# Kernel optimization log

Hardware: AMD Instinct MI355X
Metric: run time of the kernel (lower is better)

## Reference

```python
import jax, jax.numpy as jnp
import numpy as np

T, D, I, E, K = 2048, 2048, 5632, 8, 2


def setup_inputs() -> dict:
    key = jax.random.key(0)
    k1, k2, k3, k4, k5 = jax.random.split(key, 5)
    s = 0.02
    return {
        "x": jax.random.normal(k1, (T, D), dtype=jnp.float32),
        "gate_w": jax.random.normal(k2, (E, D), dtype=jnp.float32) * s,
        "w_gate": jax.random.normal(k3, (E, I, D), dtype=jnp.float32) * s,
        "w_up": jax.random.normal(k4, (E, I, D), dtype=jnp.float32) * s,
        "w_down": jax.random.normal(k5, (E, D, I), dtype=jnp.float32) * s,
    }


def reference(x, gate_w, w_gate, w_up, w_down):
    # Router: logits [T, E], top-k then softmax over the k selected logits
    logits = x @ gate_w.T
    top_vals, top_idx = jax.lax.top_k(logits, K)          # [T, K]
    rw = jax.nn.softmax(top_vals, axis=-1)                # [T, K]
    # Dense combine weights [T, E]: sum of routing weights over selected slots.
    # Mathematically identical to the per-(expert, slot) scatter-add in torch,
    # since duplicate selections of the same expert just sum their weights.
    combine = jnp.sum(jax.nn.one_hot(top_idx, E, dtype=x.dtype) * rw[..., None], axis=1)  # [T, E]
    # SwiGLU expert MLPs, batched over experts (grouped GEMM as dense einsum)
    g = jnp.einsum("td,eid->tei", x, w_gate)              # [T, E, I]
    u = jnp.einsum("td,eid->tei", x, w_up)                # [T, E, I]
    h = jax.nn.silu(g) * u                                 # [T, E, I]
    out_e = jnp.einsum("tei,edi->ted", h, w_down)         # [T, E, D]
    return jnp.einsum("ted,te->td", out_e, combine)       # [T, D]
```

## Files before the change

kernel.cpp:

```cpp
#include <hip/hip_runtime.h>
#include <hip/hip_bf16.h>
#include <stdint.h>

#define TTOK 2048
#define DDIM 2048
#define IDIM 5632
#define NEXP 8

typedef __attribute__((ext_vector_type(8))) short bf16x8;
typedef __attribute__((ext_vector_type(4))) float f32x4;
typedef __attribute__((ext_vector_type(8))) unsigned short u16x8;
typedef __attribute__((ext_vector_type(4))) unsigned short u16x4;

__device__ __forceinline__ unsigned short f2bf(float f) {
  union { float f; uint32_t u; } v; v.f = f;
  uint32_t u = v.u + 0x7fffu + ((v.u >> 16) & 1u);
  return (unsigned short)(u >> 16);
}

__device__ __forceinline__ uint32_t fbits(float f) {
  union { float f; uint32_t u; } v; v.f = f; return v.u;
}

__device__ __forceinline__ u16x8 cvt8t(float4 a, float4 b) {
  union { u16x8 v; uint32_t w[4]; } r;
  r.w[0] = __builtin_amdgcn_perm(fbits(a.y), fbits(a.x), 0x07060302);
  r.w[1] = __builtin_amdgcn_perm(fbits(a.w), fbits(a.z), 0x07060302);
  r.w[2] = __builtin_amdgcn_perm(fbits(b.y), fbits(b.x), 0x07060302);
  r.w[3] = __builtin_amdgcn_perm(fbits(b.w), fbits(b.z), 0x07060302);
  return r.v;
}

typedef __attribute__((address_space(3))) void lds_t;
typedef const __attribute__((address_space(1))) void gbl_t;
__device__ __forceinline__ void gload16(const void* g, void* l) {
  __builtin_amdgcn_global_load_lds((gbl_t*)g, (lds_t*)l, 16, 0, 0);
}

#define PIPE_BAR1() asm volatile("s_waitcnt vmcnt(12) lgkmcnt(0)\n\ts_barrier" ::: "memory")
#define PIPE_BAR2() asm volatile("s_barrier" ::: "memory")

__global__ __launch_bounds__(256) void router_kernel(
    const float* __restrict__ x, const float* __restrict__ gw,
    unsigned short* __restrict__ xbf,
    int* __restrict__ cnt, int* __restrict__ slots, float* __restrict__ wts)
{
  const int lane = threadIdx.x & 63;
  const int t = (blockIdx.x * blockDim.x + threadIdx.x) >> 6;
  const float* xr = x + (size_t)t * DDIM;
  float acc[NEXP];
#pragma unroll
  for (int e = 0; e < NEXP; ++e) acc[e] = 0.f;
#pragma unroll
  for (int it = 0; it < DDIM / 256; ++it) {
    const int d = (it * 64 + lane) * 4;
    const float4 xv = *(const float4*)(xr + d);
    u16x4 xb; xb[0]=f2bf(xv.x); xb[1]=f2bf(xv.y); xb[2]=f2bf(xv.z); xb[3]=f2bf(xv.w);
    *(u16x4*)(xbf + (size_t)t * DDIM + d) = xb;
#pragma unroll
    for (int e = 0; e < NEXP; ++e) {
      const float4 gv = *(const float4*)(gw + (size_t)e * DDIM + d);
      acc[e] += xv.x*gv.x + xv.y*gv.y + xv.z*gv.z + xv.w*gv.w;
    }
  }
#pragma unroll
  for (int e = 0; e < NEXP; ++e) {
    float v = acc[e];
#pragma unroll
    for (int off = 32; off > 0; off >>= 1) v += __shfl_xor(v, off);
    acc[e] = v;
  }
  if (lane == 0) {
    int i0 = 0; float v0 = acc[0];
#pragma unroll
    for (int e = 1; e < NEXP; ++e) if (acc[e] > v0) { v0 = acc[e]; i0 = e; }
    int i1 = -1; float v1 = -3.4e38f;
#pragma unroll
    for (int e = 0; e < NEXP; ++e) { if (e == i0) continue; if (acc[e] > v1) { v1 = acc[e]; i1 = e; } }
    const float e1 = __expf(v1 - v0);
    const float w0 = 1.f / (1.f + e1);
    const float w1 = e1 / (1.f + e1);
    const int p0 = atomicAdd(&cnt[i0], 1);
    slots[i0 * TTOK + p0] = t * 2;     wts[i0 * TTOK + p0] = w0;
    const int p1 = atomicAdd(&cnt[i1], 1);
    slots[i1 * TTOK + p1] = t * 2 + 1; wts[i1 * TTOK + p1] = w1;
  }
}

__global__ void plan_kernel(const int* __restrict__ cnt,
                            int* __restrict__ tilemap, int* __restrict__ ntiles)
{
  if (threadIdx.x == 0 && blockIdx.x == 0) {
    int n = 0;
#pragma unroll
    for (int e = 0; e < NEXP; ++e) {
      const int nt = (cnt[e] + 127) >> 7;
      for (int m = 0; m < nt; ++m) tilemap[n++] = (e << 8) | m;
    }
    ntiles[0] = n;
  }
}


__global__ __launch_bounds__(256) void gateup_kernel(
    const unsigned short* __restrict__ xbf,
    const float* __restrict__ wg, const float* __restrict__ wu,
    const int* __restrict__ cnt, const int* __restrict__ slots,
    const int* __restrict__ tilemap, const int* __restrict__ ntiles,
    unsigned short* __restrict__ h)
{
  const int flat = (blockIdx.x & 7) * 440 + (blockIdx.x >> 3);
  const int ti = flat % 40;
  if (ti >= ntiles[0]) return;
  const int em = tilemap[ti];
  const int e = em >> 8;
  const int mt = em & 255;
  const int n0 = (flat / 40) * 64;
  const int count = cnt[e];
  const int m0 = mt * 128;

  __shared__ unsigned short A[2][128][64];
  __shared__ unsigned short Bg[64][64];
  __shared__ unsigned short Bu[64][64];
  __shared__ int rslot[128];
  __shared__ int rtok[128];

  const int tid = threadIdx.x;
  const int lane = tid & 63;
  const int wid = tid >> 6;

  if (tid < 128) {
    const int idx = m0 + tid;
    const int safe = slots[e * TTOK + m0];
    const int s = (idx < count) ? slots[e * TTOK + idx] : safe;
    rslot[tid] = (idx < count) ? s : -1;
    rtok[tid] = s >> 1;
  }
  __syncthreads();

  const int aswz = ((lane & 7) ^ ((lane >> 3) & 7)) * 8;
  const unsigned short* aptr[4];
#pragma unroll
  for (int j = 0; j < 4; ++j) {
    const int arow = wid * 32 + j * 8 + (lane >> 3);
    aptr[j] = xbf + (size_t)rtok[arow] * DDIM + aswz;
  }

  const int brow = tid >> 2;
  const int bcb = (tid & 3) * 2;
  const int bswz = brow & 7;
  const size_t wboff = (size_t)e * IDIM * DDIM + (size_t)(n0 + brow) * DDIM + bcb * 8;
  const float* gsrc = wg + wboff;
  const float* usrc = wu + wboff;

  const int wr = wid >> 1, wc = wid & 1;
  const int fr = lane & 15;
  const int kc = lane >> 4;
  const int rsw = fr & 7;

  f32x4 accg[4][2] = {};
  f32x4 accu[4][2] = {};

#pragma unroll
  for (int j = 0; j < 4; ++j) gload16(aptr[j], &A[0][wid * 32][0] + j * 512);
  float4 pg4[4], pu4[4];
#pragma unroll
  for (int q = 0; q < 4; ++q) { pg4[q] = *(const float4*)(gsrc + q * 4); pu4[q] = *(const float4*)(usrc + q * 4); }

#pragma unroll 2
  for (int t = 0; t < 32; ++t) {
    const int cur = t & 1;
    const int kp = (t < 31) ? (t + 1) * 64 : 31 * 64;

#pragma unroll
    for (int j = 0; j < 4; ++j) gload16(aptr[j] + kp, &A[cur ^ 1][wid * 32][0] + j * 512);
    float4 ng4[4], nu4[4];
#pragma unroll
    for (int q = 0; q < 4; ++q) { ng4[q] = *(const float4*)(gsrc + kp + q * 4); nu4[q] = *(const float4*)(usrc + kp + q * 4); }
    __builtin_amdgcn_sched_barrier(0);
#pragma unroll
    for (int qq = 0; qq < 2; ++qq) {
      const int oc = ((bcb + qq) ^ bswz) * 8;
      *(u16x8*)&Bg[brow][oc] = cvt8t(pg4[qq * 2], pg4[qq * 2 + 1]);
      *(u16x8*)&Bu[brow][oc] = cvt8t(pu4[qq * 2], pu4[qq * 2 + 1]);
    }
    PIPE_BAR1();

    __builtin_amdgcn_s_setprio(1);
#pragma unroll
    for (int kk = 0; kk < 2; ++kk) {
      bf16x8 a[4], bg[2], bu[2];
      const int cs = ((kk * 4 + kc) ^ rsw) * 8;
#pragma unroll
      for (int mf = 0; mf < 4; ++mf)
        a[mf] = *(const bf16x8*)&A[cur][wr * 64 + mf * 16 + fr][cs];
#pragma unroll
      for (int nf = 0; nf < 2; ++nf) {
        bg[nf] = *(const bf16x8*)&Bg[wc * 32 + nf * 16 + fr][cs];
        bu[nf] = *(const bf16x8*)&Bu[wc * 32 + nf * 16 + fr][cs];
      }
#pragma unroll
      for (int mf = 0; mf < 4; ++mf)
#pragma unroll
        for (int nf = 0; nf < 2; ++nf) {
          accg[mf][nf] = __builtin_amdgcn_mfma_f32_16x16x32_bf16(a[mf], bg[nf], accg[mf][nf], 0, 0, 0);
          accu[mf][nf] = __builtin_amdgcn_mfma_f32_16x16x32_bf16(a[mf], bu[nf], accu[mf][nf], 0, 0, 0);
        }
    }
    __builtin_amdgcn_s_setprio(0);

    PIPE_BAR2();

#pragma unroll
    for (int q = 0; q < 4; ++q) { pg4[q] = ng4[q]; pu4[q] = nu4[q]; }
  }

#pragma unroll
  for (int mf = 0; mf < 4; ++mf)
#pragma unroll
    for (int nf = 0; nf < 2; ++nf)
#pragma unroll
      for (int j = 0; j < 4; ++j) {
        const int r = wr * 64 + mf * 16 + (lane >> 4) * 4 + j;
        const int s = rslot[r];
        if (s >= 0) {
          const float g = accg[mf][nf][j];
          const float u = accu[mf][nf][j];
          const float hv = g / (1.f + __expf(-g)) * u;
          h[(size_t)s * IDIM + n0 + wc * 32 + nf * 16 + fr] = f2bf(hv);
        }
      }
}

__global__ __launch_bounds__(256) void down_kernel(
    const unsigned short* __restrict__ h,
    const float* __restrict__ wd,
    const int* __restrict__ cnt, const int* __restrict__ slots,
    const float* __restrict__ wts,
    const int* __restrict__ tilemap, const int* __restrict__ ntiles,
    float* __restrict__ out)
{
  const int flat = (blockIdx.x & 7) * 160 + (blockIdx.x >> 3);
  const int ti = flat % 40;
  if (ti >= ntiles[0]) return;
  const int em = tilemap[ti];
  const int e = em >> 8;
  const int mt = em & 255;
  const int r2 = flat / 40;
  const int n0 = (r2 & 15) * 128;
  const int ks = r2 >> 4;
  const int kbase = ks * (IDIM / 2);
  const int count = cnt[e];
  const int m0 = mt * 128;

  __shared__ unsigned short A[2][128][64];
  __shared__ unsigned short B[128][64];
  __shared__ int rslot[128];
  __shared__ float rw[128];

  const int tid = threadIdx.x;
  const int lane = tid & 63;
  const int wid = tid >> 6;

  if (tid < 128) {
    const int idx = m0 + tid;
    const int safe = slots[e * TTOK + m0];
    const int s = (idx < count) ? slots[e * TTOK + idx] : safe;
    rslot[tid] = (idx < count) ? s : (safe | 0x40000000);
    rw[tid] = (idx < count) ? wts[e * TTOK + idx] : 0.f;
  }
  __syncthreads();

  const int aswz = ((lane & 7) ^ ((lane >> 3) & 7)) * 8;
  const unsigned short* aptr[4];
#pragma unroll
  for (int j = 0; j < 4; ++j) {
    const int arow = wid * 32 + j * 8 + (lane >> 3);
    aptr[j] = h + (size_t)(rslot[arow] & 0x3fffffff) * IDIM + kbase + aswz;
  }

  const int brow = tid >> 1;
  const int bcb = (tid & 1) * 4;
  const int bswz = brow & 7;
  const float* bsrc = wd + (size_t)e * DDIM * IDIM + (size_t)(n0 + brow) * IDIM + kbase + bcb * 8;

  const int wr = wid >> 1, wc = wid & 1;
  const int fr = lane & 15;
  const int kc = lane >> 4;
  const int rsw = fr & 7;

  f32x4 acc[4][4] = {};

#pragma unroll
  for (int j = 0; j < 4; ++j) gload16(aptr[j], &A[0][wid * 32][0] + j * 512);
  float4 pb4[8];
#pragma unroll
  for (int q = 0; q < 8; ++q) pb4[q] = *(const float4*)(bsrc + q * 4);

#pragma unroll 2
  for (int t = 0; t < 44; ++t) {
    const int cur = t & 1;
    const int kp = (t < 43) ? (t + 1) * 64 : 43 * 64;

#pragma unroll
    for (int j = 0; j < 4; ++j) gload16(aptr[j] + kp, &A[cur ^ 1][wid * 32][0] + j * 512);
    float4 nb4[8];
#pragma unroll
    for (int q = 0; q < 8; ++q) nb4[q] = *(const float4*)(bsrc + kp + q * 4);
    __builtin_amdgcn_sched_barrier(0);
#pragma unroll
    for (int qq = 0; qq < 4; ++qq)
      *(u16x8*)&B[brow][((bcb + qq) ^ bswz) * 8] = cvt8t(pb4[qq * 2], pb4[qq * 2 + 1]);
    PIPE_BAR1();

    __builtin_amdgcn_s_setprio(1);
#pragma unroll
    for (int kk = 0; kk < 2; ++kk) {
      bf16x8 a[4], b[4];
      const int cs = ((kk * 4 + kc) ^ rsw) * 8;
#pragma unroll
      for (int mf = 0; mf < 4; ++mf)
        a[mf] = *(const bf16x8*)&A[cur][wr * 64 + mf * 16 + fr][cs];
#pragma unroll
      for (int nf = 0; nf < 4; ++nf)
        b[nf] = *(const bf16x8*)&B[wc * 64 + nf * 16 + fr][cs];
#pragma unroll
      for (int mf = 0; mf < 4; ++mf)
#pragma unroll
        for (int nf = 0; nf < 4; ++nf)
          acc[mf][nf] = __builtin_amdgcn_mfma_f32_16x16x32_bf16(a[mf], b[nf], acc[mf][nf], 0, 0, 0);
    }
    __builtin_amdgcn_s_setprio(0);

    PIPE_BAR2();

#pragma unroll
    for (int q = 0; q < 8; ++q) pb4[q] = nb4[q];
  }

#pragma unroll
  for (int mf = 0; mf < 4; ++mf)
#pragma unroll
    for (int j = 0; j < 4; ++j) {
      const int r = wr * 64 + mf * 16 + (lane >> 4) * 4 + j;
      const int s = rslot[r];
      if (!(s & 0x40000000)) {
        const int t2 = s >> 1;
        const float w = rw[r];
#pragma unroll
        for (int nf = 0; nf < 4; ++nf)
          atomicAdd(out + (size_t)t2 * DDIM + n0 + wc * 64 + nf * 16 + fr,
                    acc[mf][nf][j] * w);
      }
    }
}

extern "C" void kernel_launch(void* const* d_in, const int* in_sizes, int n_in,
                              void* d_out, int out_size, void* d_ws, size_t ws_size,
                              hipStream_t stream) {
  const float* x  = (const float*)d_in[0];
  const float* gw = (const float*)d_in[1];
  const float* wg = (const float*)d_in[2];
  const float* wu = (const float*)d_in[3];
  const float* wd = (const float*)d_in[4];
  float* out = (float*)d_out;

  char* ws = (char*)d_ws;
  unsigned short* xbf = (unsigned short*)ws;
  unsigned short* h   = (unsigned short*)(ws + 8388608);
  int*   slots = (int*)(ws + 8388608 + 46137344);
  float* wts   = (float*)(ws + 8388608 + 46137344 + 65536);
  int*   cnt   = (int*)(ws + 8388608 + 46137344 + 131072);
  int*   tmap  = (int*)(ws + 8388608 + 46137344 + 131072 + 32);
  int*   ntl   = (int*)(ws + 8388608 + 46137344 + 131072 + 288);

  hipMemsetAsync(cnt, 0, NEXP * sizeof(int), stream);
  hipMemsetAsync(d_out, 0, (size_t)TTOK * DDIM * sizeof(float), stream);

  router_kernel<<<TTOK / 4, 256, 0, stream>>>(x, gw, xbf, cnt, slots, wts);
  plan_kernel<<<1, 64, 0, stream>>>(cnt, tmap, ntl);
  gateup_kernel<<<3520, 256, 0, stream>>>(xbf, wg, wu, cnt, slots, tmap, ntl, h);
  down_kernel<<<1280, 256, 0, stream>>>(h, wd, cnt, slots, wts, tmap, ntl, out);
}
```

Measured before the change: 889.9 us.

## Shrink K-tiles, double-buffer B, and stage fp32 down weights via direct LDS loads

The gate/up kernel moves to 32-wide K tiles with double-buffered A and B shared-memory tiles. Weight register prefetch now runs two steps ahead, with a vmcnt(4) barrier, and occupancy is hinted to 3 blocks per CU. The down kernel halves its N tile to 64 and doubles the grid. It loads fp32 w_down straight into LDS with global_load_lds and converts to bf16 when reading fragments, with occupancy hinted to 4. The aim is smaller per-block LDS and registers for more resident waves, better latency hiding, and less register staging, at the cost of more barriers per unit of work and more atomic-add traffic from the larger grid.

```diff
diff --git a/kernel.cpp b/kernel.cpp
--- a/kernel.cpp
+++ b/kernel.cpp
@@ -37,8 +37,8 @@
   __builtin_amdgcn_global_load_lds((gbl_t*)g, (lds_t*)l, 16, 0, 0);
 }
 
-#define PIPE_BAR1() asm volatile("s_waitcnt vmcnt(12) lgkmcnt(0)\n\ts_barrier" ::: "memory")
-#define PIPE_BAR2() asm volatile("s_barrier" ::: "memory")
+#define GU_BAR() asm volatile("s_waitcnt vmcnt(4) lgkmcnt(0)\n\ts_barrier" ::: "memory")
+#define DN_BAR() asm volatile("s_waitcnt vmcnt(0) lgkmcnt(0)\n\ts_barrier" ::: "memory")
 
 __global__ __launch_bounds__(256) void router_kernel(
     const float* __restrict__ x, const float* __restrict__ gw,
@@ -102,7 +102,7 @@
 }
 
 
-__global__ __launch_bounds__(256) void gateup_kernel(
+__global__ __launch_bounds__(256, 3) void gateup_kernel(
     const unsigned short* __restrict__ xbf,
     const float* __restrict__ wg, const float* __restrict__ wu,
     const int* __restrict__ cnt, const int* __restrict__ slots,
@@ -119,9 +119,9 @@
   const int count = cnt[e];
   const int m0 = mt * 128;
 
-  __shared__ unsigned short A[2][128][64];
-  __shared__ unsigned short Bg[64][64];
-  __shared__ unsigned short Bu[64][64];
+  __shared__ unsigned short A[2][128][32];
+  __shared__ unsigned short Bg[2][64][32];
+  __shared__ unsigned short Bu[2][64][32];
   __shared__ int rslot[128];
   __shared__ int rtok[128];
 
@@ -138,81 +138,76 @@
   }
   __syncthreads();
 
-  const int aswz = ((lane & 7) ^ ((lane >> 3) & 7)) * 8;
-  const unsigned short* aptr[4];
-#pragma unroll
-  for (int j = 0; j < 4; ++j) {
-    const int arow = wid * 32 + j * 8 + (lane >> 3);
-    aptr[j] = xbf + (size_t)rtok[arow] * DDIM + aswz;
+  const unsigned short* aptr[2];
+#pragma unroll
+  for (int j = 0; j < 2; ++j) {
+    const int arow = wid * 32 + j * 16 + (lane >> 2);
+    aptr[j] = xbf + (size_t)rtok[arow] * DDIM + (((lane & 3) ^ (arow & 3)) * 8);
   }
 
   const int brow = tid >> 2;
-  const int bcb = (tid & 3) * 2;
-  const int bswz = brow & 7;
-  const size_t wboff = (size_t)e * IDIM * DDIM + (size_t)(n0 + brow) * DDIM + bcb * 8;
-  const float* gsrc = wg + wboff;
-  const float* usrc = wu + wboff;
+  const int lc = tid & 3;
+  const int bslot = lc ^ (brow & 3);
+  const size_t wo = (size_t)e * IDIM * DDIM + (size_t)(n0 + brow) * DDIM + lc * 8;
+  const float* gsrc = wg + wo;
+  const float* usrc = wu + wo;
 
   const int wr = wid >> 1, wc = wid & 1;
   const int fr = lane & 15;
   const int kc = lane >> 4;
-  const int rsw = fr & 7;
 
   f32x4 accg[4][2] = {};
   f32x4 accu[4][2] = {};
 
-#pragma unroll
-  for (int j = 0; j < 4; ++j) gload16(aptr[j], &A[0][wid * 32][0] + j * 512);
-  float4 pg4[4], pu4[4];
-#pragma unroll
-  for (int q = 0; q < 4; ++q) { pg4[q] = *(const float4*)(gsrc + q * 4); pu4[q] = *(const float4*)(usrc + q * 4); }
+  float4 Pg[2], Pu[2];
+  gload16(aptr[0], &A[0][wid * 32][0]);
+  gload16(aptr[1], &A[0][wid * 32 + 16][0]);
+  Pg[0] = *(const float4*)(gsrc);     Pg[1] = *(const float4*)(gsrc + 4);
+  Pu[0] = *(const float4*)(usrc);     Pu[1] = *(const float4*)(usrc + 4);
+  *(u16x8*)&Bg[0][brow][bslot * 8] = cvt8t(Pg[0], Pg[1]);
+  *(u16x8*)&Bu[0][brow][bslot * 8] = cvt8t(Pu[0], Pu[1]);
+  Pg[0] = *(const float4*)(gsrc + 32); Pg[1] = *(const float4*)(gsrc + 36);
+  Pu[0] = *(const float4*)(usrc + 32); Pu[1] = *(const float4*)(usrc + 36);
+  GU_BAR();
 
 #pragma unroll 2
-  for (int t = 0; t < 32; ++t) {
+  for (int t = 0; t < 64; ++t) {
     const int cur = t & 1;
-    const int kp = (t < 31) ? (t + 1) * 64 : 31 * 64;
-
-#pragma unroll
-    for (int j = 0; j < 4; ++j) gload16(aptr[j] + kp, &A[cur ^ 1][wid * 32][0] + j * 512);
-    float4 ng4[4], nu4[4];
-#pragma unroll
-    for (int q = 0; q < 4; ++q) { ng4[q] = *(const float4*)(gsrc + kp + q * 4); nu4[q] = *(const float4*)(usrc + kp + q * 4); }
+    const int kpA = ((t + 1 < 64) ? t + 1 : 63) * 32;
+    const int kpB = ((t + 2 < 64) ? t + 2 : 63) * 32;
+
+    gload16(aptr[0] + kpA, &A[cur ^ 1][wid * 32][0]);
+    gload16(aptr[1] + kpA, &A[cur ^ 1][wid * 32 + 16][0]);
     __builtin_amdgcn_sched_barrier(0);
-#pragma unroll
-    for (int qq = 0; qq < 2; ++qq) {
-      const int oc = ((bcb + qq) ^ bswz) * 8;
-      *(u16x8*)&Bg[brow][oc] = cvt8t(pg4[qq * 2], pg4[qq * 2 + 1]);
-      *(u16x8*)&Bu[brow][oc] = cvt8t(pu4[qq * 2], pu4[qq * 2 + 1]);
-    }
-    PIPE_BAR1();
+    *(u16x8*)&Bg[cur ^ 1][brow][bslot * 8] = cvt8t(Pg[0], Pg[1]);
+    *(u16x8*)&Bu[cur ^ 1][brow][bslot * 8] = cvt8t(Pu[0], Pu[1]);
+    Pg[0] = *(const float4*)(gsrc + kpB);     Pg[1] = *(const float4*)(gsrc + kpB + 4);
+    Pu[0] = *(const float4*)(usrc + kpB);     Pu[1] = *(const float4*)(usrc + kpB + 4);
+    __builtin_amdgcn_sched_barrier(0);
 
     __builtin_amdgcn_s_setprio(1);
-#pragma unroll
-    for (int kk = 0; kk < 2; ++kk) {
-      bf16x8 a[4], bg[2], bu[2];
-      const int cs = ((kk * 4 + kc) ^ rsw) * 8;
-#pragma unroll
-      for (int mf = 0; mf < 4; ++mf)
-        a[mf] = *(const bf16x8*)&A[cur][wr * 64 + mf * 16 + fr][cs];
+    bf16x8 a[4], bg[2], bu[2];
+#pragma unroll
+    for (int mf = 0; mf < 4; ++mf) {
+      const int r = wr * 64 + mf * 16 + fr;
+      a[mf] = *(const bf16x8*)&A[cur][r][(kc ^ (r & 3)) * 8];
+    }
+#pragma unroll
+    for (int nf = 0; nf < 2; ++nf) {
+      const int rb = wc * 32 + nf * 16 + fr;
+      bg[nf] = *(const bf16x8*)&Bg[cur][rb][(kc ^ (rb & 3)) * 8];
+      bu[nf] = *(const bf16x8*)&Bu[cur][rb][(kc ^ (rb & 3)) * 8];
+    }
+#pragma unroll
+    for (int mf = 0; mf < 4; ++mf)
 #pragma unroll
       for (int nf = 0; nf < 2; ++nf) {
-        bg[nf] = *(const bf16x8*)&Bg[wc * 32 + nf * 16 + fr][cs];
-        bu[nf] = *(const bf16x8*)&Bu[wc * 32 + nf * 16 + fr][cs];
+        accg[mf][nf] = __builtin_amdgcn_mfma_f32_16x16x32_bf16(a[mf], bg[nf], accg[mf][nf], 0, 0, 0);
+        accu[mf][nf] = __builtin_amdgcn_mfma_f32_16x16x32_bf16(a[mf], bu[nf], accu[mf][nf], 0, 0, 0);
       }
-#pragma unroll
-      for (int mf = 0; mf < 4; ++mf)
-#pragma unroll
-        for (int nf = 0; nf < 2; ++nf) {
-          accg[mf][nf] = __builtin_amdgcn_mfma_f32_16x16x32_bf16(a[mf], bg[nf], accg[mf][nf], 0, 0, 0);
-          accu[mf][nf] = __builtin_amdgcn_mfma_f32_16x16x32_bf16(a[mf], bu[nf], accu[mf][nf], 0, 0, 0);
-        }
-    }
     __builtin_amdgcn_s_setprio(0);
 
-    PIPE_BAR2();
-
-#pragma unroll
-    for (int q = 0; q < 4; ++q) { pg4[q] = ng4[q]; pu4[q] = nu4[q]; }
+    GU_BAR();
   }
 
 #pragma unroll
@@ -232,7 +227,7 @@
       }
 }
 
-__global__ __launch_bounds__(256) void down_kernel(
+__global__ __launch_bounds__(256, 4) void down_kernel(
     const unsigned short* __restrict__ h,
     const float* __restrict__ wd,
     const int* __restrict__ cnt, const int* __restrict__ slots,
@@ -240,21 +235,20 @@
     const int* __restrict__ tilemap, const int* __restrict__ ntiles,
     float* __restrict__ out)
 {
-  const int flat = (blockIdx.x & 7) * 160 + (blockIdx.x >> 3);
+  const int flat = (blockIdx.x & 7) * 320 + (blockIdx.x >> 3);
   const int ti = flat % 40;
   if (ti >= ntiles[0]) return;
   const int em = tilemap[ti];
   const int e = em >> 8;
   const int mt = em & 255;
-  const int r2 = flat / 40;
-  const int n0 = (r2 & 15) * 128;
-  const int ks = r2 >> 4;
-  const int kbase = ks * (IDIM / 2);
+  const int rest = flat / 40;
+  const int n0 = (rest & 31) * 64;
+  const int kbase = (rest >> 5) * (IDIM / 2);
   const int count = cnt[e];
   const int m0 = mt * 128;
 
-  __shared__ unsigned short A[2][128][64];
-  __shared__ unsigned short B[128][64];
+  __shared__ unsigned short A[2][128][32];
+  __shared__ float Bf[2][64][32];
   __shared__ int rslot[128];
   __shared__ float rw[128];
 
@@ -271,71 +265,69 @@
   }
   __syncthreads();
 
-  const int aswz = ((lane & 7) ^ ((lane >> 3) & 7)) * 8;
-  const unsigned short* aptr[4];
-#pragma unroll
-  for (int j = 0; j < 4; ++j) {
-    const int arow = wid * 32 + j * 8 + (lane >> 3);
-    aptr[j] = h + (size_t)(rslot[arow] & 0x3fffffff) * IDIM + kbase + aswz;
-  }
-
-  const int brow = tid >> 1;
-  const int bcb = (tid & 1) * 4;
-  const int bswz = brow & 7;
-  const float* bsrc = wd + (size_t)e * DDIM * IDIM + (size_t)(n0 + brow) * IDIM + kbase + bcb * 8;
+  const unsigned short* aptr[2];
+#pragma unroll
+  for (int j = 0; j < 2; ++j) {
+    const int arow = wid * 32 + j * 16 + (lane >> 2);
+    aptr[j] = h + (size_t)(rslot[arow] & 0x3fffffff) * IDIM + kbase
+              + (((lane & 3) ^ (arow & 3)) * 8);
+  }
+
+  const float* bptr[2];
+#pragma unroll
+  for (int j = 0; j < 2; ++j) {
+    const int browg = wid * 16 + j * 8 + (lane >> 3);
+    bptr[j] = wd + (size_t)e * DDIM * IDIM + (size_t)(n0 + browg) * IDIM + kbase
+              + (((lane & 7) ^ (browg & 7)) * 4);
+  }
 
   const int wr = wid >> 1, wc = wid & 1;
   const int fr = lane & 15;
   const int kc = lane >> 4;
-  const int rsw = fr & 7;
-
-  f32x4 acc[4][4] = {};
-
-#pragma unroll
-  for (int j = 0; j < 4; ++j) gload16(aptr[j], &A[0][wid * 32][0] + j * 512);
-  float4 pb4[8];
-#pragma unroll
-  for (int q = 0; q < 8; ++q) pb4[q] = *(const float4*)(bsrc + q * 4);
+
+  f32x4 acc[4][2] = {};
+
+  gload16(aptr[0], &A[0][wid * 32][0]);
+  gload16(aptr[1], &A[0][wid * 32 + 16][0]);
+  gload16(bptr[0], &Bf[0][wid * 16][0]);
+  gload16(bptr[1], &Bf[0][wid * 16 + 8][0]);
+  DN_BAR();
 
 #pragma unroll 2
-  for (int t = 0; t < 44; ++t) {
+  for (int t = 0; t < 88; ++t) {
     const int cur = t & 1;
-    const int kp = (t < 43) ? (t + 1) * 64 : 43 * 64;
-
-#pragma unroll
-    for (int j = 0; j < 4; ++j) gload16(aptr[j] + kp, &A[cur ^ 1][wid * 32][0] + j * 512);
-    float4 nb4[8];
-#pragma unroll
-    for (int q = 0; q < 8; ++q) nb4[q] = *(const float4*)(bsrc + kp + q * 4);
+    if (t < 87) {
+      const int kp = (t + 1) * 32;
+      gload16(aptr[0] + kp, &A[cur ^ 1][wid * 32][0]);
+      gload16(aptr[1] + kp, &A[cur ^ 1][wid * 32 + 16][0]);
+      gload16(bptr[0] + kp, &Bf[cur ^ 1][wid * 16][0]);
+      gload16(bptr[1] + kp, &Bf[cur ^ 1][wid * 16 + 8][0]);
+    }
     __builtin_amdgcn_sched_barrier(0);
-#pragma unroll
-    for (int qq = 0; qq < 4; ++qq)
-      *(u16x8*)&B[brow][((bcb + qq) ^ bswz) * 8] = cvt8t(pb4[qq * 2], pb4[qq * 2 + 1]);
-    PIPE_BAR1();
 
     __builtin_amdgcn_s_setprio(1);
-#pragma unroll
-    for (int kk = 0; kk < 2; ++kk) {
-      bf16x8 a[4], b[4];
-      const int cs = ((kk * 4 + kc) ^ rsw) * 8;
-#pragma unroll
-      for (int mf = 0; mf < 4; ++mf)
-        a[mf] = *(const bf16x8*)&A[cur][wr * 64 + mf * 16 + fr][cs];
-#pragma unroll
-      for (int nf = 0; nf < 4; ++nf)
-        b[nf] = *(const bf16x8*)&B[wc * 64 + nf * 16 + fr][cs];
-#pragma unroll
-      for (int mf = 0; mf < 4; ++mf)
-#pragma unroll
-        for (int nf = 0; nf < 4; ++nf)
-          acc[mf][nf] = __builtin_amdgcn_mfma_f32_16x16x32_bf16(a[mf], b[nf], acc[mf][nf], 0, 0, 0);
-    }
+    bf16x8 a[4], b[2];
+#pragma unroll
+    for (int mf = 0; mf < 4; ++mf) {
+      const int r = wr * 64 + mf * 16 + fr;
+      a[mf] = *(const bf16x8*)&A[cur][r][(kc ^ (r & 3)) * 8];
+    }
+#pragma unroll
+    for (int nf = 0; nf < 2; ++nf) {
+      const int rb = wc * 32 + nf * 16 + fr;
+      const int c0 = kc * 2;
+      const float4 fa = *(const float4*)&Bf[cur][rb][((c0)     ^ (rb & 7)) * 4];
+      const float4 fb = *(const float4*)&Bf[cur][rb][((c0 + 1) ^ (rb & 7)) * 4];
+      b[nf] = (bf16x8)cvt8t(fa, fb);
+    }
+#pragma unroll
+    for (int mf = 0; mf < 4; ++mf)
+#pragma unroll
+      for (int nf = 0; nf < 2; ++nf)
+        acc[mf][nf] = __builtin_amdgcn_mfma_f32_16x16x32_bf16(a[mf], b[nf], acc[mf][nf], 0, 0, 0);
     __builtin_amdgcn_s_setprio(0);
 
-    PIPE_BAR2();
-
-#pragma unroll
-    for (int q = 0; q < 8; ++q) pb4[q] = nb4[q];
+    DN_BAR();
   }
 
 #pragma unroll
@@ -348,8 +340,8 @@
         const int t2 = s >> 1;
         const float w = rw[r];
 #pragma unroll
-        for (int nf = 0; nf < 4; ++nf)
-          atomicAdd(out + (size_t)t2 * DDIM + n0 + wc * 64 + nf * 16 + fr,
+        for (int nf = 0; nf < 2; ++nf)
+          atomicAdd(out + (size_t)t2 * DDIM + n0 + wc * 32 + nf * 16 + fr,
                     acc[mf][nf][j] * w);
       }
     }
@@ -380,5 +372,5 @@
   router_kernel<<<TTOK / 4, 256, 0, stream>>>(x, gw, xbf, cnt, slots, wts);
   plan_kernel<<<1, 64, 0, stream>>>(cnt, tmap, ntl);
   gateup_kernel<<<3520, 256, 0, stream>>>(xbf, wg, wu, cnt, slots, tmap, ntl, h);
-  down_kernel<<<1280, 256, 0, stream>>>(h, wd, cnt, slots, wts, tmap, ntl, out);
-}
+  down_kernel<<<2560, 256, 0, stream>>>(h, wd, cnt, slots, wts, tmap, ntl, out);
+}
```

Result: faster. 791.8 us (-11.0%).
